# Kernel tuning notes

Hardware: AMD Instinct MI355X
Metric: run time of the kernel (lower is better)

## Reference

```python
import jax, jax.numpy as jnp
import numpy as np

# ---- hyperparameters (from args defaults) ----
TEMPERATURE = 0.07
ALPHA = 0.5
OT_EPSILON = 0.1
OT_ITERS = 20
HOLO_WEIGHT = 1.0
RKD_DISTANCE_WEIGHT = 1.0
RKD_ANGLE_WEIGHT = 2.0
GLOBAL_RKD_WEIGHT = 10.0
MATRYOSHKA_DIMS = [128, 768]
MATRYOSHKA_WEIGHTS = [1.0, 2.0]

B, N, H_S, H_T, D_REP = 64, 256, 768, 1024, 768


def l2norm(x, axis=-1):
    # F.normalize(p=2): x / max(||x||, eps)
    n = jnp.sqrt(jnp.sum(x * x, axis=axis, keepdims=True))
    return x / jnp.maximum(n, 1e-12)


def pairwise_distance(x):
    # [n, d] -> [n, n] squared-euclidean-style distances
    sq = jnp.sum(x * x, axis=1, keepdims=True)
    return sq + sq.T - 2.0 * (x @ x.T)


def huber(diff):
    a = jnp.abs(diff)
    return jnp.where(a < 1.0, 0.5 * a * a, a - 0.5)


def rkd_distance_loss(s, t):
    n = s.shape[0]
    mask = jnp.triu(jnp.ones((n, n), dtype=bool), k=1)
    cnt = jnp.sum(mask.astype(s.dtype))
    ds, dt = pairwise_distance(s), pairwise_distance(t)
    mean_s = jax.lax.stop_gradient(jnp.sum(jnp.where(mask, ds, 0.0)) / cnt) + 1e-8
    mean_t = jax.lax.stop_gradient(jnp.sum(jnp.where(mask, dt, 0.0)) / cnt) + 1e-8
    loss = huber(ds / mean_s - dt / mean_t)
    return jnp.sum(jnp.where(mask, loss, 0.0)) / cnt


def angle_potentials(x):
    # diffs[i, j] = x[j] - x[i]
    diffs = x[None, :, :] - x[:, None, :]
    e = diffs / (jnp.linalg.norm(diffs, axis=-1, keepdims=True) + 1e-8)
    return jnp.einsum('ijd,kjd->ijk', e, e)


def rkd_angle_loss(s, t):
    psi_s, psi_t = angle_potentials(s), angle_potentials(t)
    n = psi_s.shape[0]
    idx = jnp.arange(n)
    i, j, k = idx[:, None, None], idx[None, :, None], idx[None, None, :]
    mask = (i != j) & (i != k) & (j != k)  # exclude degenerate triplets
    cnt = jnp.sum(mask.astype(s.dtype))
    loss = huber(psi_s - psi_t)
    return jnp.sum(jnp.where(mask, loss, 0.0)) / cnt


def saliency_measure(h, temp=1.0):
    # softmax over token axis of hidden-state norms -> [B, N, 1]
    norms = jnp.linalg.norm(h, axis=-1)
    return jax.nn.softmax(norms / temp, axis=-1)[..., None]


def structure_matrix(z):
    zn = l2norm(z, axis=-1)
    return 1.0 - jnp.einsum('bnd,bmd->bnm', zn, zn)


def sinkhorn_knopp_log_domain(C, mu, nu):
    # C: [B, Ns, Nt]; mu: [B, Ns, 1]; nu: [B, Nt, 1]
    log_K = -C / OT_EPSILON
    log_mu = jnp.log(mu + 1e-8)
    log_nu = jnp.log(nu + 1e-8)
    u = jnp.zeros_like(mu)
    v = jnp.zeros_like(nu)
    for _ in range(OT_ITERS):
        u = log_mu - jax.scipy.special.logsumexp(
            log_K + jnp.swapaxes(v, 1, 2), axis=2, keepdims=True)
        v = log_nu - jax.scipy.special.logsumexp(
            jnp.swapaxes(log_K, 1, 2) + jnp.swapaxes(u, 1, 2),
            axis=2, keepdims=True)
    return jnp.exp(u + log_K + jnp.swapaxes(v, 1, 2))


def fused_gromov_wasserstein(z_s, z_t, proj_w, proj_b):
    mu = saliency_measure(z_s)   # [B, N, 1]
    nu = saliency_measure(z_t)   # [B, N, 1]
    C_s = structure_matrix(z_s)  # [B, N, N]
    C_t = structure_matrix(z_t)
    z_s_norm = l2norm(z_s @ proj_w + proj_b, axis=-1)
    z_t_norm = l2norm(z_t, axis=-1)
    M = 1.0 - jnp.einsum('bnd,bmd->bnm', z_s_norm, z_t_norm)
    Gamma = sinkhorn_knopp_log_domain(M, mu, nu)
    feat_loss = jnp.mean(jnp.sum(M * Gamma, axis=(1, 2)))
    Gamma_norm = Gamma / (jnp.sum(Gamma, axis=2, keepdims=True) + 1e-8)
    C_t_mapped = jnp.einsum('bnm,bmk,blk->bnl', Gamma_norm, C_t, Gamma_norm)
    w = jnp.einsum('bni,bmi->bnm', mu, mu)  # mu @ mu^T
    struct_loss = jnp.mean(jnp.sum((C_s - C_t_mapped) ** 2 * w, axis=(1, 2)))
    return (1.0 - ALPHA) * feat_loss + ALPHA * struct_loss


def cross_entropy_inbatch(scores):
    # labels = arange(B)
    logZ = jax.scipy.special.logsumexp(scores, axis=1)
    return jnp.mean(logZ - jnp.diagonal(scores))


def setup_inputs() -> dict:
    key = jax.random.key(0)
    ks = jax.random.split(key, 10)
    return {
        's_q_reps': jax.random.normal(ks[0], (B, D_REP), jnp.float32),
        's_p_reps': jax.random.normal(ks[1], (B, D_REP), jnp.float32),
        't_q_reps': jax.random.normal(ks[2], (B, D_REP), jnp.float32),
        't_p_reps': jax.random.normal(ks[3], (B, D_REP), jnp.float32),
        's_q_states': jax.random.normal(ks[4], (B, N, H_S), jnp.float32),
        's_p_states': jax.random.normal(ks[5], (B, N, H_S), jnp.float32),
        't_q_states': jax.random.normal(ks[6], (B, N, H_T), jnp.float32),
        't_p_states': jax.random.normal(ks[7], (B, N, H_T), jnp.float32),
        'proj_w': jax.random.normal(ks[8], (H_S, H_T), jnp.float32) * (H_S ** -0.5),
        'proj_b': jnp.zeros((H_T,), jnp.float32),
    }


def reference(s_q_reps, s_p_reps, t_q_reps, t_p_reps,
              s_q_states, s_p_states, t_q_states, t_p_states,
              proj_w, proj_b):
    # teacher outputs are computed under torch.no_grad()
    t_q_reps = jax.lax.stop_gradient(t_q_reps)
    t_p_reps = jax.lax.stop_gradient(t_p_reps)
    t_q_states = jax.lax.stop_gradient(t_q_states)
    t_p_states = jax.lax.stop_gradient(t_p_states)

    contrastive_acc = 0.0
    holo_acc = 0.0
    rkd_acc = 0.0
    for dim, dim_weight in zip(MATRYOSHKA_DIMS, MATRYOSHKA_WEIGHTS):
        s_q_slice = l2norm(s_q_reps[:, :dim])
        s_p_slice = l2norm(s_p_reps[:, :dim])
        scores = (s_q_slice @ s_p_slice.T) / TEMPERATURE
        contrastive_acc += dim_weight * cross_entropy_inbatch(scores)
        if dim <= 128:
            s_batch = jnp.concatenate([s_q_slice, s_p_slice], axis=0)
            t_batch = jnp.concatenate(
                [l2norm(t_q_reps[:, :dim]), l2norm(t_p_reps[:, :dim])], axis=0)
            loss_dist = rkd_distance_loss(s_batch, t_batch)
            loss_angle = rkd_angle_loss(s_batch, t_batch)
            rkd_val = (RKD_DISTANCE_WEIGHT * loss_dist
                       + RKD_ANGLE_WEIGHT * loss_angle)
            rkd_acc += GLOBAL_RKD_WEIGHT * rkd_val * 2.0
        else:
            loss_q = fused_gromov_wasserstein(s_q_states, t_q_states, proj_w, proj_b)
            loss_p = fused_gromov_wasserstein(s_p_states, t_p_states, proj_w, proj_b)
            holo_acc += HOLO_WEIGHT * 0.5 * (loss_q + loss_p)
    return contrastive_acc + holo_acc + rkd_acc
```

## Files before the change

kernel.cpp:

```cpp
#include <hip/hip_runtime.h>
#include <math.h>

#define NB   64
#define NN   256
#define HSS  768
#define HTT  1024
#define ROWS (NB*NN)
#define C2LOG 14.426950408889634f

typedef unsigned short u16;
typedef __attribute__((ext_vector_type(8))) short bf16x8;
typedef __attribute__((ext_vector_type(4))) float f32x4;

#define LIDX(r,c) (((r)<<8) + (((((c)>>3) + (r)) & 31)<<3) + ((c)&7))
#define EIDX(r,c) (((r)<<7) + (((((c)>>3) + (r)) & 15)<<3) + ((c)&7))

__device__ __forceinline__ void gl16(const u16* g, u16* l){
  __builtin_amdgcn_global_load_lds(
      (const __attribute__((address_space(1))) unsigned int*)g,
      (__attribute__((address_space(3))) unsigned int*)l,
      16, 0, 0);
}

static const size_t OFF_ACC   = 0;
static const size_t OFF_SQ128 = 16;
static const size_t OFF_SP128 = OFF_SQ128 + 64*128;
static const size_t OFF_TQ128 = OFF_SP128 + 64*128;
static const size_t OFF_TP128 = OFF_TQ128 + 64*128;
static const size_t OFF_SQ768 = OFF_TP128 + 64*128;
static const size_t OFF_SP768 = OFF_SQ768 + 64*768;
static const size_t OFF_DS    = OFF_SP768 + 64*768;
static const size_t OFF_DT    = OFF_DS + 128*128;
static const size_t OFF_CS    = OFF_DT + 128*128;
static const size_t OFF_MBF   = OFF_CS  + (size_t)2*NB*NN*NN;
static const size_t OFF_ZS_BF = OFF_MBF + (size_t)NB*NN*NN;
static const size_t OFF_ZT_BF = OFF_ZS_BF + (size_t)ROWS*HSS/2;
static const size_t OFF_WT_BF = OFF_ZT_BF + (size_t)ROWS*HTT/2;
static const size_t OFF_ZSP_BF= OFF_WT_BF + (size_t)HTT*HSS/2;
static const size_t OFF_GN_BF = OFF_ZSP_BF+ (size_t)ROWS*HTT/2;
static const size_t OFF_CT_BF = OFF_GN_BF + (size_t)NB*NN*NN;
static const size_t OFF_T_BF  = OFF_ZS_BF;
static const size_t OFF_NS    = OFF_CT_BF + (size_t)NB*NN*NN;
static const size_t OFF_NT    = OFF_NS + ROWS;
static const size_t OFF_NSP   = OFF_NT + ROWS;
static const size_t OFF_MU    = OFF_NSP + ROWS;
static const size_t OFF_NU    = OFF_MU + 2*ROWS;


__device__ __forceinline__ float wred_sum(float v){
  #pragma unroll
  for(int o=32;o>0;o>>=1) v += __shfl_xor(v,o,64);
  return v;
}
__device__ __forceinline__ float wred_max(float v){
  #pragma unroll
  for(int o=32;o>0;o>>=1) v = fmaxf(v, __shfl_xor(v,o,64));
  return v;
}
__device__ __forceinline__ u16 f2bf(float f){
  unsigned u = __float_as_uint(f);
  unsigned r = (u + 0x7fffu + ((u>>16)&1u)) >> 16;
  return (u16)r;
}
__device__ __forceinline__ float bf2f(u16 h){
  return __uint_as_float(((unsigned)h)<<16);
}

__global__ __launch_bounds__(256) void k_l2norm_all(
    const float* __restrict__ sq, const float* __restrict__ sp,
    const float* __restrict__ tq, const float* __restrict__ tp,
    float* __restrict__ ws){
  int bid = blockIdx.x;
  int r = bid & 63;
  const float* in; float* out; int kuse;
  if(bid < 64)       { in = sq; out = ws + OFF_SQ128; kuse = 128; }
  else if(bid < 128) { in = sp; out = ws + OFF_SP128; kuse = 128; }
  else if(bid < 192) { in = tq; out = ws + OFF_TQ128; kuse = 128; }
  else if(bid < 256) { in = tp; out = ws + OFF_TP128; kuse = 128; }
  else if(bid < 320) { in = sq; out = ws + OFF_SQ768; kuse = 768; }
  else               { in = sp; out = ws + OFF_SP768; kuse = 768; }
  const float* row = in + (size_t)r*768;
  float ss = 0.f;
  for(int d=threadIdx.x; d<kuse; d+=256){ float x=row[d]; ss += x*x; }
  ss = wred_sum(ss);
  __shared__ float sm[4];
  if((threadIdx.x&63)==0) sm[threadIdx.x>>6]=ss;
  __syncthreads();
  float tot = sm[0]+sm[1]+sm[2]+sm[3];
  float inv = 1.f / fmaxf(sqrtf(tot), 1e-12f);
  for(int d=threadIdx.x; d<kuse; d+=256) out[(size_t)r*kuse + d] = row[d]*inv;
}

__global__ __launch_bounds__(512) void k_contrastive2(const float* __restrict__ ws,
    float* __restrict__ acc){
  int bid = blockIdx.x;
  int i = bid & 63;
  int big = bid >> 6;
  const float* q = ws + (big ? OFF_SQ768 : OFF_SQ128);
  const float* p = ws + (big ? OFF_SP768 : OFF_SP128);
  int dim = big ? 768 : 128;
  float weight = big ? 2.f : 1.f;
  int j = threadIdx.x & 63;
  int part = threadIdx.x >> 6;
  const float* qi = q + (size_t)i*dim;
  const float* pj = p + (size_t)j*dim;
  int seg = dim >> 3;
  int d0 = part*seg;
  float dot = 0.f;
  for(int d=d0; d<d0+seg; d+=4){
    float4 a = *(const float4*)(qi+d);
    float4 b = *(const float4*)(pj+d);
    dot = fmaf(a.x,b.x,dot);
    dot = fmaf(a.y,b.y,dot);
    dot = fmaf(a.z,b.z,dot);
    dot = fmaf(a.w,b.w,dot);
  }
  __shared__ float sm[8][64];
  sm[part][j] = dot;
  __syncthreads();
  if(part==0){
    float s = 0.f;
    #pragma unroll
    for(int k=0;k<8;k++) s += sm[k][j];
    s = s / 0.07f;
    float mx = wred_max(s);
    float e = expf(s - mx);
    float Z = wred_sum(e);
    float logZ = mx + logf(Z);
    float diag = __shfl(s, i, 64);
    if(j==0) atomicAdd(acc+0, weight*(logZ - diag)*(1.f/64.f));
  }
}

__global__ __launch_bounds__(256) void k_pack_cvt(
    const float* __restrict__ zs, const float* __restrict__ zt,
    u16* __restrict__ zsb, u16* __restrict__ ztb,
    float* __restrict__ ns, float* __restrict__ nt,
    const float* __restrict__ sb128, const float* __restrict__ tb128,
    float* __restrict__ ds, float* __restrict__ dt, float* __restrict__ acc)
{
  __shared__ float sm[2][2];
  int bid = blockIdx.x;
  if(bid < 8192){
    const float* in; u16* out; float* nrm; int K; int cb;
    if(bid < 4096){ in=zs; out=zsb; nrm=ns; K=HSS; cb=bid; }
    else          { in=zt; out=ztb; nrm=nt; K=HTT; cb=bid-4096; }
    int w = threadIdx.x >> 6, l = threadIdx.x & 63;
    int r = cb*4 + w;
    const float* row = in + (size_t)r*K;
    u16* orow = out + (size_t)r*K;
    float ss = 0.f;
    int nv = K >> 8;
    for(int i=0;i<nv;i++){
      int d = l*4 + i*256;
      float4 x = *(const float4*)(row + d);
      ushort4 o; o.x=f2bf(x.x); o.y=f2bf(x.y); o.z=f2bf(x.z); o.w=f2bf(x.w);
      *(ushort4*)(orow + d) = o;
      ss += x.x*x.x + x.y*x.y + x.z*x.z + x.w*x.w;
    }
    ss = wred_sum(ss);
    if(l==0) nrm[r] = sqrtf(ss);
    return;
  }
  {
    int r = bid - 8192;
    int c = threadIdx.x;
    float ms = 0.f, mt = 0.f;
    if(c < 128){
      const float* sr = sb128 + r*128; const float* sc = sb128 + c*128;
      const float* tr = tb128 + r*128; const float* tc = tb128 + c*128;
      float dot_s=0,ssr=0,ssc=0,dot_t=0,tsr=0,tsc=0;
      for(int d=0; d<128; d++){
        float a=sr[d], bb=sc[d]; dot_s += a*bb; ssr += a*a; ssc += bb*bb;
        float at=tr[d], bt=tc[d]; dot_t += at*bt; tsr += at*at; tsc += bt*bt;
      }
      float dv = ssr + ssc - 2.f*dot_s;
      float tv = tsr + tsc - 2.f*dot_t;
      ds[r*128+c] = dv; dt[r*128+c] = tv;
      ms = (c>r)? dv : 0.f;
      mt = (c>r)? tv : 0.f;
      ms = wred_sum(ms); mt = wred_sum(mt);
      if((c&63)==0){ sm[0][c>>6]=ms; sm[1][c>>6]=mt; }
    }
    __syncthreads();
    if(threadIdx.x==0){
      atomicAdd(acc+1, sm[0][0]+sm[0][1]);
      atomicAdd(acc+2, sm[1][0]+sm[1][1]);
    }
  }
}

__global__ __launch_bounds__(256) void k_small0(
    const float* __restrict__ ds, const float* __restrict__ dt,
    const float* __restrict__ ns, const float* __restrict__ nt,
    float* __restrict__ omu, float* __restrict__ onu, float* __restrict__ acc)
{
  __shared__ float sm[4], sm2[4];
  int bid = blockIdx.x;
  if(bid < 128){
    int r = bid, c = threadIdx.x;
    float mean_s = acc[1]*(1.f/8128.f) + 1e-8f;
    float mean_t = acc[2]*(1.f/8128.f) + 1e-8f;
    float h = 0.f;
    if(c < 128){
      if(c > r){
        float diff = ds[r*128+c]/mean_s - dt[r*128+c]/mean_t;
        float a = fabsf(diff);
        h = (a<1.f)? 0.5f*a*a : a-0.5f;
      }
      h = wred_sum(h);
      if((c&63)==0) sm[c>>6]=h;
    }
    __syncthreads();
    if(threadIdx.x==0) atomicAdd(acc+3, sm[0]+sm[1]);
    return;
  }
  {
    int b0 = bid - 128, n = threadIdx.x;
    const float* nrm = (b0 < NB) ? ns : nt;
    float* out = (b0 < NB) ? omu : onu;
    int b = b0 & 63;
    float x = nrm[b*NN+n];
    float mx = wred_max(x);
    if((n&63)==0) sm[n>>6]=mx;
    __syncthreads();
    mx = fmaxf(fmaxf(sm[0],sm[1]),fmaxf(sm[2],sm[3]));
    float e = expf(x-mx);
    float s = wred_sum(e);
    if((n&63)==0) sm2[n>>6]=s;
    __syncthreads();
    s = sm2[0]+sm2[1]+sm2[2]+sm2[3];
    out[b*NN+n] = e/s;
  }
}

#define RKD_LDS 65536
__global__ __launch_bounds__(256, 1) void k_rkd_angle_mfma(
    const float* __restrict__ sb, const float* __restrict__ tb,
    float* __restrict__ accp)
{
  extern __shared__ u16 eSh[];
  u16* Es = eSh;
  u16* Et = eSh + 128*128;
  const int j    = blockIdx.x >> 1;
  const int half = blockIdx.x & 1;
  const int tid = threadIdx.x;
  {
    const int i = tid >> 1, h = tid & 1;
    #pragma unroll
    for(int which=0; which<2; which++){
      const float* xb = which ? tb : sb;
      u16* E = which ? Et : Es;
      const float* xj = xb + j*128 + h*64;
      const float* xi = xb + i*128 + h*64;
      float ss = 0.f;
      #pragma unroll
      for(int d4=0; d4<16; d4++){
        float4 a = *(const float4*)(xj + d4*4);
        float4 b = *(const float4*)(xi + d4*4);
        float d0=a.x-b.x, d1=a.y-b.y, d2=a.z-b.z, d3=a.w-b.w;
        ss += d0*d0+d1*d1+d2*d2+d3*d3;
      }
      ss += __shfl_xor(ss, 1, 64);
      float inv = (i==j) ? 0.f : 1.f/(sqrtf(ss)+1e-8f);
      #pragma unroll
      for(int d4=0; d4<16; d4++){
        float4 a = *(const float4*)(xj + d4*4);
        float4 b = *(const float4*)(xi + d4*4);
        int c = h*64 + d4*4;
        E[EIDX(i,c+0)] = f2bf((a.x-b.x)*inv);
        E[EIDX(i,c+1)] = f2bf((a.y-b.y)*inv);
        E[EIDX(i,c+2)] = f2bf((a.z-b.z)*inv);
        E[EIDX(i,c+3)] = f2bf((a.w-b.w)*inv);
      }
    }
  }
  __syncthreads();
  const int w = tid >> 6, lane = tid & 63;
  const int q = lane >> 4, loc = lane & 15;
  float hsum = 0.f;
  #pragma unroll
  for(int ni=0; ni<4; ni++){
    const int cb = half*64 + ni*16;
    #pragma unroll
    for(int mi=0; mi<2; mi++){
      const int rb = w*32 + mi*16;
      f32x4 as_ = {0.f,0.f,0.f,0.f}, at_ = {0.f,0.f,0.f,0.f};
      #pragma unroll
      for(int k0=0; k0<128; k0+=32){
        int ra = rb + loc, rbn = cb + loc;
        int ca = k0 + q*8;
        bf16x8 aS = *(const bf16x8*)(Es + EIDX(ra, ca));
        bf16x8 bS = *(const bf16x8*)(Es + EIDX(rbn, ca));
        bf16x8 aT = *(const bf16x8*)(Et + EIDX(ra, ca));
        bf16x8 bT = *(const bf16x8*)(Et + EIDX(rbn, ca));
        as_ = __builtin_amdgcn_mfma_f32_16x16x32_bf16(aS, bS, as_, 0,0,0);
        at_ = __builtin_amdgcn_mfma_f32_16x16x32_bf16(aT, bT, at_, 0,0,0);
      }
      #pragma unroll
      for(int jj=0; jj<4; jj++){
        int row = rb + q*4 + jj, col = cb + loc;
        if(row != col){
          float d = as_[jj] - at_[jj];
          float a = fabsf(d);
          hsum += (a < 1.f) ? 0.5f*a*a : a - 0.5f;
        }
      }
    }
  }
  hsum = wred_sum(hsum);
  __syncthreads();
  float* red = (float*)eSh;
  if(lane==0) red[w] = hsum;
  __syncthreads();
  if(tid==0) atomicAdd(accp+4, red[0]+red[1]+red[2]+red[3]);
}

__global__ __launch_bounds__(256) void k_row_norm_bf16(const u16* __restrict__ z,
    float* __restrict__ nrm, int K){
  int w = threadIdx.x >> 6, l = threadIdx.x & 63;
  int r = blockIdx.x*4 + w;
  const u16* row = z + (size_t)r*K;
  float ss = 0.f;
  int nv = K >> 9;
  for(int i=0;i<nv;i++){
    int d = l*8 + i*512;
    uint4 v = *(const uint4*)(row + d);
    float a0=__uint_as_float(v.x<<16), a1=__uint_as_float(v.x&0xffff0000u);
    float a2=__uint_as_float(v.y<<16), a3=__uint_as_float(v.y&0xffff0000u);
    float a4=__uint_as_float(v.z<<16), a5=__uint_as_float(v.z&0xffff0000u);
    float a6=__uint_as_float(v.w<<16), a7=__uint_as_float(v.w&0xffff0000u);
    ss += a0*a0+a1*a1+a2*a2+a3*a3+a4*a4+a5*a5+a6*a6+a7*a7;
  }
  ss = wred_sum(ss);
  if(l==0) nrm[r] = sqrtf(ss);
}

__global__ void k_wt(const float* __restrict__ W, u16* __restrict__ Wt){
  __shared__ float t[32][33];
  int k0 = blockIdx.y*32, n0 = blockIdx.x*32;
  int tx = threadIdx.x, ty = threadIdx.y;
  for(int r=0;r<32;r+=8) t[ty+r][tx] = W[(size_t)(k0+ty+r)*HTT + n0+tx];
  __syncthreads();
  for(int r=0;r<32;r+=8) Wt[(size_t)(n0+ty+r)*HSS + k0+tx] = f2bf(t[tx][ty+r]);
}

__global__ __launch_bounds__(256) void k_saliency2(const float* __restrict__ ns,
    const float* __restrict__ nt, float* __restrict__ omu, float* __restrict__ onu){
  int b0 = blockIdx.x, n = threadIdx.x;
  const float* nrm = (b0 < NB) ? ns : nt;
  float* out = (b0 < NB) ? omu : onu;
  int b = b0 & 63;
  float x = nrm[b*NN+n];
  float mx = wred_max(x);
  __shared__ float sm[4], sm2[4];
  if((n&63)==0) sm[n>>6]=mx;
  __syncthreads();
  mx = fmaxf(fmaxf(sm[0],sm[1]),fmaxf(sm[2],sm[3]));
  float e = expf(x-mx);
  float s = wred_sum(e);
  if((n&63)==0) sm2[n>>6]=s;
  __syncthreads();
  s = sm2[0]+sm2[1]+sm2[2]+sm2[3];
  out[b*NN+n] = e/s;
}

enum { MODE_PROJ=0, MODE_COST=1, MODE_PLAIN=2, MODE_STRUCT=3 };

template<int MODE>
__global__ __launch_bounds__(256) void k_mfma(
    const u16* __restrict__ A, int lda, long bA,
    const u16* __restrict__ B, int ldb, long bB,
    int K,
    float* __restrict__ outF, u16* __restrict__ outB, int ldo, long bO,
    const float* __restrict__ nx, const float* __restrict__ ny,
    const float* __restrict__ bias,
    const float* __restrict__ Cs, const float* __restrict__ mu,
    float* __restrict__ accp)
{
  __shared__ u16 As[128*32];
  __shared__ u16 Bs[128*32];
  __shared__ float red[4];

  int gx = gridDim.x, gy = gridDim.y;
  int flat = blockIdx.x + gx*(blockIdx.y + gy*blockIdx.z);
  int nwg  = gx*gy*gridDim.z;
  int cpx  = nwg >> 3;
  int lg   = (flat & 7)*cpx + (flat >> 3);
  int bx   = lg % gx;
  int rest = lg / gx;
  int by   = rest % gy;
  int b    = rest / gy;

  const u16* Ab = A + (size_t)b*bA;
  const u16* Bb = B + (size_t)b*bB;
  int tid = threadIdx.x;
  int lane = tid & 63, w = tid >> 6;
  int m0 = by*128, n0 = bx*128;
  int row_off = (w>>1)*64, col_off = (w&1)*64;
  int q = lane>>4, loc = lane&15;
  f32x4 acc[4][4] = {};

  const int srow = (lane >> 2);
  const int sslot = lane & 3;

  for(int k0=0;k0<K;k0+=32){
    #pragma unroll
    for(int h=0;h<2;h++){
      int row = h*64 + w*16 + srow;
      int ca  = (sslot ^ ((row>>1)&3))*8;
      u16* ldst = As + h*2048 + w*512 + lane*8;
      u16* ldstB= Bs + h*2048 + w*512 + lane*8;
      gl16(Ab + (size_t)(m0+row)*lda + k0 + ca, ldst);
      gl16(Bb + (size_t)(n0+row)*ldb + k0 + ca, ldstB);
    }
    __syncthreads();
    bf16x8 af[4], bfr[4];
    #pragma unroll
    for(int mi=0;mi<4;mi++){
      int r = row_off + mi*16 + loc;
      int slot = q ^ ((r>>1)&3);
      af[mi] = *(const bf16x8*)(As + r*32 + slot*8);
    }
    #pragma unroll
    for(int ni=0;ni<4;ni++){
      int r = col_off + ni*16 + loc;
      int slot = q ^ ((r>>1)&3);
      bfr[ni] = *(const bf16x8*)(Bs + r*32 + slot*8);
    }
    #pragma unroll
    for(int mi=0;mi<4;mi++)
      #pragma unroll
      for(int ni=0;ni<4;ni++)
        acc[mi][ni] = __builtin_amdgcn_mfma_f32_16x16x32_bf16(af[mi], bfr[ni], acc[mi][ni], 0,0,0);
    __syncthreads();
  }

  float* outFb = outF ? outF + (size_t)b*bO : nullptr;
  u16*   outBb = outB ? outB + (size_t)b*bO : nullptr;
  const float* nxb = nx ? nx + (size_t)b*NN : nullptr;
  const float* nyb = ny ? ny + (size_t)b*NN : nullptr;
  const float* Cb  = (MODE==MODE_STRUCT) ? Cs + (size_t)b*bO : nullptr;
  const float* mb  = (MODE==MODE_STRUCT) ? mu + (size_t)b*NN : nullptr;
  float lsum = 0.f;
  #pragma unroll
  for(int mi=0;mi<4;mi++){
    #pragma unroll
    for(int j=0;j<4;j++){
      int row = m0 + row_off + mi*16 + q*4 + j;
      float ir = 0.f, mr = 0.f;
      if(MODE==MODE_COST)   ir = 1.f/fmaxf(nxb[row],1e-12f);
      if(MODE==MODE_STRUCT) mr = mb[row];
      #pragma unroll
      for(int ni=0;ni<4;ni++){
        int col = n0 + col_off + ni*16 + loc;
        float v = acc[mi][ni][j];
        if(MODE==MODE_PROJ){
          v += bias[col];
          outBb[(size_t)row*ldo + col] = f2bf(v);
        } else if(MODE==MODE_COST){
          float ic = 1.f/fmaxf(nyb[col],1e-12f);
          v = 1.f - v*ir*ic;
          if(outFb) outFb[(size_t)row*ldo + col] = v;
          if(outBb) outBb[(size_t)row*ldo + col] = f2bf(v);
        } else if(MODE==MODE_PLAIN){
          outBb[(size_t)row*ldo + col] = f2bf(v);
        } else {
          float d = Cb[(size_t)row*ldo + col] - v;
          lsum += d*d*mr*mb[col];
        }
      }
    }
  }
  if(MODE==MODE_STRUCT){
    lsum = wred_sum(lsum);
    if(lane==0) red[w] = lsum;
    __syncthreads();
    if(tid==0) atomicAdd(accp+6, red[0]+red[1]+red[2]+red[3]);
  }
}

template<int MODE>
__global__ __launch_bounds__(256) void k_mfma64(
    const u16* __restrict__ A, int lda, long bA,
    const u16* __restrict__ B, int ldb, long bB,
    int K,
    float* __restrict__ outF, u16* __restrict__ outB, int ldo, long bO,
    const float* __restrict__ nx, const float* __restrict__ ny,
    const float* __restrict__ bias,
    const float* __restrict__ Cs, const float* __restrict__ mu,
    float* __restrict__ accp)
{
  __shared__ u16 As[64*32];
  __shared__ u16 Bs[64*32];
  __shared__ float red[4];

  int gx = gridDim.x, gy = gridDim.y;
  int flat = blockIdx.x + gx*(blockIdx.y + gy*blockIdx.z);
  int nwg  = gx*gy*gridDim.z;
  int cpx  = nwg >> 3;
  int lg   = (flat & 7)*cpx + (flat >> 3);
  int bx   = lg % gx;
  int rest = lg / gx;
  int by   = rest % gy;
  int b    = rest / gy;

  const u16* Ab = A + (size_t)b*bA;
  const u16* Bb = B + (size_t)b*bB;
  int tid = threadIdx.x;
  int lane = tid & 63, w = tid >> 6;
  int m0 = by*64, n0 = bx*64;
  int row_off = (w>>1)*32, col_off = (w&1)*32;
  int q = lane>>4, loc = lane&15;
  f32x4 acc[2][2] = {};

  const int srow = tid >> 2;
  const int sslot = tid & 3;

  for(int k0=0;k0<K;k0+=32){
    {
      int row = srow;
      int ca  = (sslot ^ ((row>>1)&3))*8;
      u16* la = As + w*512 + lane*8;
      u16* lb = Bs + w*512 + lane*8;
      gl16(Ab + (size_t)(m0+row)*lda + k0 + ca, la);
      gl16(Bb + (size_t)(n0+row)*ldb + k0 + ca, lb);
    }
    __syncthreads();
    bf16x8 af[2], bfr[2];
    #pragma unroll
    for(int mi=0;mi<2;mi++){
      int r = row_off + mi*16 + loc;
      int slot = q ^ ((r>>1)&3);
      af[mi] = *(const bf16x8*)(As + r*32 + slot*8);
    }
    #pragma unroll
    for(int ni=0;ni<2;ni++){
      int r = col_off + ni*16 + loc;
      int slot = q ^ ((r>>1)&3);
      bfr[ni] = *(const bf16x8*)(Bs + r*32 + slot*8);
    }
    #pragma unroll
    for(int mi=0;mi<2;mi++)
      #pragma unroll
      for(int ni=0;ni<2;ni++)
        acc[mi][ni] = __builtin_amdgcn_mfma_f32_16x16x32_bf16(af[mi], bfr[ni], acc[mi][ni], 0,0,0);
    __syncthreads();
  }

  float* outFb = outF ? outF + (size_t)b*bO : nullptr;
  u16*   outBb = outB ? outB + (size_t)b*bO : nullptr;
  const float* nxb = nx ? nx + (size_t)b*NN : nullptr;
  const float* nyb = ny ? ny + (size_t)b*NN : nullptr;
  const float* Cb  = (MODE==MODE_STRUCT) ? Cs + (size_t)b*bO : nullptr;
  const float* mb  = (MODE==MODE_STRUCT) ? mu + (size_t)b*NN : nullptr;
  float lsum = 0.f;
  #pragma unroll
  for(int mi=0;mi<2;mi++){
    #pragma unroll
    for(int j=0;j<4;j++){
      int row = m0 + row_off + mi*16 + q*4 + j;
      float ir = 0.f, mr = 0.f;
      if(MODE==MODE_COST)   ir = 1.f/fmaxf(nxb[row],1e-12f);
      if(MODE==MODE_STRUCT) mr = mb[row];
      #pragma unroll
      for(int ni=0;ni<2;ni++){
        int col = n0 + col_off + ni*16 + loc;
        float v = acc[mi][ni][j];
        if(MODE==MODE_PROJ){
          v += bias[col];
          outBb[(size_t)row*ldo + col] = f2bf(v);
        } else if(MODE==MODE_COST){
          float ic = 1.f/fmaxf(nyb[col],1e-12f);
          v = 1.f - v*ir*ic;
          if(outFb) outFb[(size_t)row*ldo + col] = v;
          if(outBb) outBb[(size_t)row*ldo + col] = f2bf(v);
        } else if(MODE==MODE_PLAIN){
          outBb[(size_t)row*ldo + col] = f2bf(v);
        } else {
          float d = Cb[(size_t)row*ldo + col] - v;
          lsum += d*d*mr*mb[col];
        }
      }
    }
  }
  if(MODE==MODE_STRUCT){
    lsum = wred_sum(lsum);
    if(lane==0) red[w] = lsum;
    __syncthreads();
    if(tid==0) atomicAdd(accp+6, red[0]+red[1]+red[2]+red[3]);
  }
}

__global__ __launch_bounds__(256) void k_mfma64_dual(
    const u16* __restrict__ A1, const u16* __restrict__ A2,
    const u16* __restrict__ B, int ld, long bStr,
    int K,
    u16* __restrict__ out1, u16* __restrict__ out2, long bO,
    const float* __restrict__ n1, const float* __restrict__ n2,
    const float* __restrict__ ny)
{
  __shared__ u16 A1s[64*32];
  __shared__ u16 A2s[64*32];
  __shared__ u16 Bs[64*32];

  int gx = gridDim.x, gy = gridDim.y;
  int flat = blockIdx.x + gx*(blockIdx.y + gy*blockIdx.z);
  int nwg  = gx*gy*gridDim.z;
  int cpx  = nwg >> 3;
  int lg   = (flat & 7)*cpx + (flat >> 3);
  int bx   = lg % gx;
  int rest = lg / gx;
  int by   = rest % gy;
  int b    = rest / gy;

  const u16* A1b = A1 + (size_t)b*bStr;
  const u16* A2b = A2 + (size_t)b*bStr;
  const u16* Bb  = B  + (size_t)b*bStr;
  int tid = threadIdx.x;
  int lane = tid & 63, w = tid >> 6;
  int m0 = by*64, n0 = bx*64;
  int row_off = (w>>1)*32, col_off = (w&1)*32;
  int q = lane>>4, loc = lane&15;
  f32x4 acc1[2][2] = {};
  f32x4 acc2[2][2] = {};

  const int srow = tid >> 2;
  const int sslot = tid & 3;

  for(int k0=0;k0<K;k0+=32){
    {
      int row = srow;
      int ca  = (sslot ^ ((row>>1)&3))*8;
      u16* l1 = A1s + w*512 + lane*8;
      u16* l2 = A2s + w*512 + lane*8;
      u16* lb = Bs  + w*512 + lane*8;
      gl16(A1b + (size_t)(m0+row)*ld + k0 + ca, l1);
      gl16(A2b + (size_t)(m0+row)*ld + k0 + ca, l2);
      gl16(Bb  + (size_t)(n0+row)*ld + k0 + ca, lb);
    }
    __syncthreads();
    bf16x8 a1f[2], a2f[2], bfr[2];
    #pragma unroll
    for(int mi=0;mi<2;mi++){
      int r = row_off + mi*16 + loc;
      int slot = q ^ ((r>>1)&3);
      a1f[mi] = *(const bf16x8*)(A1s + r*32 + slot*8);
      a2f[mi] = *(const bf16x8*)(A2s + r*32 + slot*8);
    }
    #pragma unroll
    for(int ni=0;ni<2;ni++){
      int r = col_off + ni*16 + loc;
      int slot = q ^ ((r>>1)&3);
      bfr[ni] = *(const bf16x8*)(Bs + r*32 + slot*8);
    }
    #pragma unroll
    for(int mi=0;mi<2;mi++)
      #pragma unroll
      for(int ni=0;ni<2;ni++){
        acc1[mi][ni] = __builtin_amdgcn_mfma_f32_16x16x32_bf16(a1f[mi], bfr[ni], acc1[mi][ni], 0,0,0);
        acc2[mi][ni] = __builtin_amdgcn_mfma_f32_16x16x32_bf16(a2f[mi], bfr[ni], acc2[mi][ni], 0,0,0);
      }
    __syncthreads();
  }

  u16* o1 = out1 + (size_t)b*bO;
  u16* o2 = out2 + (size_t)b*bO;
  const float* n1b = n1 + (size_t)b*NN;
  const float* n2b = n2 + (size_t)b*NN;
  const float* nyb = ny + (size_t)b*NN;
  #pragma unroll
  for(int mi=0;mi<2;mi++){
    #pragma unroll
    for(int j=0;j<4;j++){
      int row = m0 + row_off + mi*16 + q*4 + j;
      float ir1 = 1.f/fmaxf(n1b[row],1e-12f);
      float ir2 = 1.f/fmaxf(n2b[row],1e-12f);
      #pragma unroll
      for(int ni=0;ni<2;ni++){
        int col = n0 + col_off + ni*16 + loc;
        float ic = 1.f/fmaxf(nyb[col],1e-12f);
        float v1 = 1.f - acc1[mi][ni][j]*ir1*ic;
        float v2 = 1.f - acc2[mi][ni][j]*ir2*ic;
        o1[(size_t)row*NN + col] = f2bf(v1);
        o2[(size_t)row*NN + col] = f2bf(v2);
      }
    }
  }
}

#define SINK_DYN_LDS 131072
__global__ __launch_bounds__(1024, 1) void k_sinkhorn_fused(
    const u16* __restrict__ Mbf, const float* __restrict__ muL,
    const float* __restrict__ nuL, u16* __restrict__ Gn, float* __restrict__ accp)
{
  extern __shared__ u16 Ks[];
  __shared__ __align__(16) float part[4096];
  __shared__ __align__(16) float su[NN], sv[NN], smu[NN], snu[NN];
  __shared__ float red[16];

  const int b = blockIdx.x;
  const int t = threadIdx.x;
  const u16* Mb = Mbf + (size_t)b*NN*NN;

  #pragma unroll
  for(int i=0;i<16;i++){
    int e = (i*1024 + t)*4;
    int r = e>>8, c = e&255;
    ushort4 mv = *(const ushort4*)(Mb + e);
    ushort4 o;
    o.x = f2bf(exp2f(-C2LOG*bf2f(mv.x)));
    o.y = f2bf(exp2f(-C2LOG*bf2f(mv.y)));
    o.z = f2bf(exp2f(-C2LOG*bf2f(mv.z)));
    o.w = f2bf(exp2f(-C2LOG*bf2f(mv.w)));
    *(ushort4*)(Ks + LIDX(r,c)) = o;
  }
  if(t < NN){
    smu[t] = muL[(size_t)b*NN+t] + 1e-8f;
    snu[t] = nuL[(size_t)b*NN+t] + 1e-8f;
    sv[t] = 1.f;
  }
  __syncthreads();

  const int r_ = t & 255, p_ = t >> 8;
  const int w = t>>6, l = t&63;

  for(int it=0; it<20; it++){
    {
      float s0=0.f, s1=0.f, s2=0.f, s3=0.f;
      #pragma unroll
      for(int jj=0;jj<8;jj++){
        int c0 = p_*64 + jj*8;
        uint4 kv = *(const uint4*)(Ks + LIDX(r_, c0));
        float4 va = *(const float4*)(sv + c0);
        float4 vb = *(const float4*)(sv + c0 + 4);
        s0 = fmaf(__uint_as_float(kv.x<<16),           va.x, s0);
        s1 = fmaf(__uint_as_float(kv.x & 0xffff0000u), va.y, s1);
        s2 = fmaf(__uint_as_float(kv.y<<16),           va.z, s2);
        s3 = fmaf(__uint_as_float(kv.y & 0xffff0000u), va.w, s3);
        s0 = fmaf(__uint_as_float(kv.z<<16),           vb.x, s0);
        s1 = fmaf(__uint_as_float(kv.z & 0xffff0000u), vb.y, s1);
        s2 = fmaf(__uint_as_float(kv.w<<16),           vb.z, s2);
        s3 = fmaf(__uint_as_float(kv.w & 0xffff0000u), vb.w, s3);
      }
      part[t] = (s0+s1)+(s2+s3);
    }
    __syncthreads();
    if(t < NN){
      float S = part[t] + part[256+t] + part[512+t] + part[768+t];
      su[t] = smu[t] / S;
    }
    __syncthreads();
    {
      float cs0=0.f,cs1=0.f,cs2=0.f,cs3=0.f;
      #pragma unroll
      for(int rr=0;rr<16;rr++){
        int r = w*16 + rr;
        ushort4 kv = *(const ushort4*)(Ks + LIDX(r, l*4));
        float ur = su[r];
        cs0 = fmaf(bf2f(kv.x), ur, cs0);
        cs1 = fmaf(bf2f(kv.y), ur, cs1);
        cs2 = fmaf(bf2f(kv.z), ur, cs2);
        cs3 = fmaf(bf2f(kv.w), ur, cs3);
      }
      float4 o; o.x=cs0; o.y=cs1; o.z=cs2; o.w=cs3;
      *(float4*)(part + w*256 + l*4) = o;
    }
    __syncthreads();
    if(t < NN){
      float S = 0.f;
      #pragma unroll
      for(int ww=0;ww<16;ww++) S += part[ww*256 + t];
      sv[t] = snu[t] / S;
    }
    __syncthreads();
  }

  {
    float s0=0.f, s1=0.f, s2=0.f, s3=0.f;
    #pragma unroll
    for(int jj=0;jj<8;jj++){
      int c0 = p_*64 + jj*8;
      uint4 kv = *(const uint4*)(Ks + LIDX(r_, c0));
      float4 va = *(const float4*)(sv + c0);
      float4 vb = *(const float4*)(sv + c0 + 4);
      s0 = fmaf(__uint_as_float(kv.x<<16),           va.x, s0);
      s1 = fmaf(__uint_as_float(kv.x & 0xffff0000u), va.y, s1);
      s2 = fmaf(__uint_as_float(kv.y<<16),           va.z, s2);
      s3 = fmaf(__uint_as_float(kv.y & 0xffff0000u), va.w, s3);
      s0 = fmaf(__uint_as_float(kv.z<<16),           vb.x, s0);
      s1 = fmaf(__uint_as_float(kv.z & 0xffff0000u), vb.y, s1);
      s2 = fmaf(__uint_as_float(kv.w<<16),           vb.z, s2);
      s3 = fmaf(__uint_as_float(kv.w & 0xffff0000u), vb.w, s3);
    }
    part[t] = (s0+s1)+(s2+s3);
  }
  __syncthreads();
  if(t < NN){
    float S = part[t] + part[256+t] + part[512+t] + part[768+t];
    smu[t] = 1.f / (su[t]*S + 1e-8f);
  }
  __syncthreads();

  u16* Gb = Gn + (size_t)b*NN*NN;
  const float IC = -1.f/C2LOG;
  float v0 = sv[l*4+0], v1 = sv[l*4+1], v2 = sv[l*4+2], v3 = sv[l*4+3];
  float fl = 0.f;
  for(int rr=0;rr<16;rr++){
    int r = w*16 + rr;
    ushort4 kv = *(const ushort4*)(Ks + LIDX(r, l*4));
    float k0=bf2f(kv.x), k1=bf2f(kv.y), k2=bf2f(kv.z), k3=bf2f(kv.w);
    float ur = su[r], inv = smu[r];
    float g0=ur*k0*v0, g1=ur*k1*v1, g2=ur*k2*v2, g3=ur*k3*v3;
    fl += g0*(__log2f(k0)*IC) + g1*(__log2f(k1)*IC)
        + g2*(__log2f(k2)*IC) + g3*(__log2f(k3)*IC);
    ushort4 o;
    o.x=f2bf(g0*inv); o.y=f2bf(g1*inv); o.z=f2bf(g2*inv); o.w=f2bf(g3*inv);
    *(ushort4*)(Gb + (size_t)r*NN + l*4) = o;
  }
  fl = wred_sum(fl);
  if(l==0) red[w] = fl;
  __syncthreads();
  if(t==0){
    float s=0.f;
    #pragma unroll
    for(int i=0;i<16;i++) s+=red[i];
    atomicAdd(accp+5, s);
  }
}

__global__ void k_final(const float* __restrict__ acc, float* __restrict__ out){
  out[0] = acc[0]
         + 20.f*acc[3]*(1.f/8128.f)
         + 40.f*acc[4]*(1.f/2048256.f)
         + 0.25f*(acc[5]+acc[6])*(1.f/64.f);
}

extern "C" void kernel_launch(void* const* d_in, const int* in_sizes, int n_in,
                              void* d_out, int out_size, void* d_ws, size_t ws_size,
                              hipStream_t stream) {
  const float* s_q_reps   = (const float*)d_in[0];
  const float* s_p_reps   = (const float*)d_in[1];
  const float* t_q_reps   = (const float*)d_in[2];
  const float* t_p_reps   = (const float*)d_in[3];
  const float* s_q_states = (const float*)d_in[4];
  const float* s_p_states = (const float*)d_in[5];
  const float* t_q_states = (const float*)d_in[6];
  const float* t_p_states = (const float*)d_in[7];
  const float* proj_w     = (const float*)d_in[8];
  const float* proj_b     = (const float*)d_in[9];
  float* ws = (float*)d_ws;
  float* acc = ws + OFF_ACC;
  u16* M_BF   = (u16*)(ws + OFF_MBF);
  u16* ZS_BF  = (u16*)(ws + OFF_ZS_BF);
  u16* ZT_BF  = (u16*)(ws + OFF_ZT_BF);
  u16* WT_BF  = (u16*)(ws + OFF_WT_BF);
  u16* ZSP_BF = (u16*)(ws + OFF_ZSP_BF);
  u16* GN_BF  = (u16*)(ws + OFF_GN_BF);
  u16* CT_BF  = (u16*)(ws + OFF_CT_BF);
  u16* T_BF   = (u16*)(ws + OFF_T_BF);

  hipFuncSetAttribute(reinterpret_cast<const void*>(k_sinkhorn_fused),
                      hipFuncAttributeMaxDynamicSharedMemorySize, SINK_DYN_LDS);
  hipFuncSetAttribute(reinterpret_cast<const void*>(k_rkd_angle_mfma),
                      hipFuncAttributeMaxDynamicSharedMemorySize, RKD_LDS);

  hipMemsetAsync(acc, 0, 16*sizeof(float), stream);

  k_l2norm_all<<<384,256,0,stream>>>(s_q_reps, s_p_reps, t_q_reps, t_p_reps, ws);
  k_contrastive2<<<128,512,0,stream>>>(ws, acc);

  k_pack_cvt<<<8320,256,0,stream>>>(s_q_states, t_q_states, ZS_BF, ZT_BF,
      ws+OFF_NS, ws+OFF_NT, ws+OFF_SQ128, ws+OFF_TQ128, ws+OFF_DS, ws+OFF_DT, acc);
  k_small0<<<256,256,0,stream>>>(ws+OFF_DS, ws+OFF_DT, ws+OFF_NS, ws+OFF_NT,
      ws+OFF_MU, ws+OFF_NU, acc);
  k_rkd_angle_mfma<<<256,256,RKD_LDS,stream>>>(ws+OFF_SQ128, ws+OFF_TQ128, acc);
  k_wt<<<dim3(HTT/32, HSS/32),dim3(32,8),0,stream>>>(proj_w, WT_BF);

  for(int pass=0; pass<2; pass++){
    size_t po  = (size_t)pass*NB*NN*NN;
    size_t pr  = (size_t)pass*ROWS;
    if(pass==1){
      k_pack_cvt<<<8192,256,0,stream>>>(s_p_states, t_p_states, ZS_BF, ZT_BF,
          ws+OFF_NS, ws+OFF_NT, ws+OFF_SQ128, ws+OFF_TQ128, ws+OFF_DS, ws+OFF_DT, acc);
      k_saliency2<<<128,256,0,stream>>>(ws+OFF_NS, ws+OFF_NT, ws+OFF_MU+pr, ws+OFF_NU+pr);
    }
    k_mfma<MODE_PROJ><<<dim3(HTT/128, ROWS/128, 1),256,0,stream>>>(
        ZS_BF, HSS, 0, WT_BF, HSS, 0, HSS,
        nullptr, ZSP_BF, HTT, 0,
        nullptr, nullptr, proj_b, nullptr, nullptr, nullptr);
    k_row_norm_bf16<<<ROWS/4,256,0,stream>>>(ZSP_BF, ws+OFF_NSP, HTT);
    k_mfma64<MODE_COST><<<dim3(4,4,NB),256,0,stream>>>(
        ZS_BF, HSS, (long)NN*HSS, ZS_BF, HSS, (long)NN*HSS, HSS,
        ws+OFF_CS+po, nullptr, NN, (long)NN*NN,
        ws+OFF_NS, ws+OFF_NS, nullptr, nullptr, nullptr, nullptr);
    k_mfma64_dual<<<dim3(4,4,NB),256,0,stream>>>(
        ZT_BF, ZSP_BF, ZT_BF, HTT, (long)NN*HTT, HTT,
        CT_BF+po, M_BF+po, (long)NN*NN,
        ws+OFF_NT, ws+OFF_NSP, ws+OFF_NT);
  }

  k_sinkhorn_fused<<<2*NB,1024,SINK_DYN_LDS,stream>>>(
      M_BF, ws+OFF_MU, ws+OFF_NU, GN_BF, acc);

  k_mfma64<MODE_PLAIN><<<dim3(4,4,2*NB),256,0,stream>>>(
      GN_BF, NN, (long)NN*NN, CT_BF, NN, (long)NN*NN, NN,
      nullptr, T_BF, NN, (long)NN*NN,
      nullptr, nullptr, nullptr, nullptr, nullptr, nullptr);
  k_mfma64<MODE_STRUCT><<<dim3(4,4,2*NB),256,0,stream>>>(
      T_BF, NN, (long)NN*NN, GN_BF, NN, (long)NN*NN, NN,
      nullptr, nullptr, NN, (long)NN*NN,
      nullptr, nullptr, nullptr, ws+OFF_CS, ws+OFF_MU, acc);

  k_final<<<1,1,0,stream>>>(acc, (float*)d_out);
}
```

Measured before the change: 603.1 us.

## Fuse projection row norms into projection GEMM and overlap pass-1 cost GEMM with Sinkhorn

The projection GEMM now writes per-slice partial sums of squares of its bf16 outputs, which replaces the separate row-norm kernel. The dual GEMM sums the 16 partials to get each row norm. The pass-1 student cost-matrix GEMM moves into extra blocks of the Sinkhorn launch (384 blocks instead of 128), so it runs alongside the 128 Sinkhorn blocks rather than as its own launch. The intent is to drop a kernel launch and a re-read of the projected matrix, and to fill idle CUs during Sinkhorn. The cost is that 1024-thread blocks with large LDS doing small GEMMs may use those CUs inefficiently.

```diff
diff --git a/kernel.cpp b/kernel.cpp
--- a/kernel.cpp
+++ b/kernel.cpp
@@ -42,9 +42,9 @@
 static const size_t OFF_T_BF  = OFF_ZS_BF;
 static const size_t OFF_NS    = OFF_CT_BF + (size_t)NB*NN*NN;
 static const size_t OFF_NT    = OFF_NS + ROWS;
-static const size_t OFF_NSP   = OFF_NT + ROWS;
-static const size_t OFF_MU    = OFF_NSP + ROWS;
+static const size_t OFF_MU    = OFF_NT + ROWS;
 static const size_t OFF_NU    = OFF_MU + 2*ROWS;
+static const size_t OFF_NSPP  = OFF_NU + 2*ROWS;
 
 
 __device__ __forceinline__ float wred_sum(float v){
@@ -316,26 +316,6 @@
   if(tid==0) atomicAdd(accp+4, red[0]+red[1]+red[2]+red[3]);
 }
 
-__global__ __launch_bounds__(256) void k_row_norm_bf16(const u16* __restrict__ z,
-    float* __restrict__ nrm, int K){
-  int w = threadIdx.x >> 6, l = threadIdx.x & 63;
-  int r = blockIdx.x*4 + w;
-  const u16* row = z + (size_t)r*K;
-  float ss = 0.f;
-  int nv = K >> 9;
-  for(int i=0;i<nv;i++){
-    int d = l*8 + i*512;
-    uint4 v = *(const uint4*)(row + d);
-    float a0=__uint_as_float(v.x<<16), a1=__uint_as_float(v.x&0xffff0000u);
-    float a2=__uint_as_float(v.y<<16), a3=__uint_as_float(v.y&0xffff0000u);
-    float a4=__uint_as_float(v.z<<16), a5=__uint_as_float(v.z&0xffff0000u);
-    float a6=__uint_as_float(v.w<<16), a7=__uint_as_float(v.w&0xffff0000u);
-    ss += a0*a0+a1*a1+a2*a2+a3*a3+a4*a4+a5*a5+a6*a6+a7*a7;
-  }
-  ss = wred_sum(ss);
-  if(l==0) nrm[r] = sqrtf(ss);
-}
-
 __global__ void k_wt(const float* __restrict__ W, u16* __restrict__ Wt){
   __shared__ float t[32][33];
   int k0 = blockIdx.y*32, n0 = blockIdx.x*32;
@@ -365,35 +345,22 @@
   out[b*NN+n] = e/s;
 }
 
-enum { MODE_PROJ=0, MODE_COST=1, MODE_PLAIN=2, MODE_STRUCT=3 };
-
-template<int MODE>
-__global__ __launch_bounds__(256) void k_mfma(
-    const u16* __restrict__ A, int lda, long bA,
-    const u16* __restrict__ B, int ldb, long bB,
-    int K,
-    float* __restrict__ outF, u16* __restrict__ outB, int ldo, long bO,
-    const float* __restrict__ nx, const float* __restrict__ ny,
-    const float* __restrict__ bias,
-    const float* __restrict__ Cs, const float* __restrict__ mu,
-    float* __restrict__ accp)
+__global__ __launch_bounds__(256) void k_proj(
+    const u16* __restrict__ A, const u16* __restrict__ B,
+    u16* __restrict__ outB, const float* __restrict__ bias,
+    float* __restrict__ nspp)
 {
   __shared__ u16 As[128*32];
   __shared__ u16 Bs[128*32];
-  __shared__ float red[4];
 
   int gx = gridDim.x, gy = gridDim.y;
-  int flat = blockIdx.x + gx*(blockIdx.y + gy*blockIdx.z);
-  int nwg  = gx*gy*gridDim.z;
+  int flat = blockIdx.x + gx*blockIdx.y;
+  int nwg  = gx*gy;
   int cpx  = nwg >> 3;
   int lg   = (flat & 7)*cpx + (flat >> 3);
   int bx   = lg % gx;
-  int rest = lg / gx;
-  int by   = rest % gy;
-  int b    = rest / gy;
-
-  const u16* Ab = A + (size_t)b*bA;
-  const u16* Bb = B + (size_t)b*bB;
+  int by   = lg / gx;
+
   int tid = threadIdx.x;
   int lane = tid & 63, w = tid >> 6;
   int m0 = by*128, n0 = bx*128;
@@ -404,15 +371,15 @@
   const int srow = (lane >> 2);
   const int sslot = lane & 3;
 
-  for(int k0=0;k0<K;k0+=32){
+  for(int k0=0;k0<HSS;k0+=32){
     #pragma unroll
     for(int h=0;h<2;h++){
       int row = h*64 + w*16 + srow;
       int ca  = (sslot ^ ((row>>1)&3))*8;
       u16* ldst = As + h*2048 + w*512 + lane*8;
       u16* ldstB= Bs + h*2048 + w*512 + lane*8;
-      gl16(Ab + (size_t)(m0+row)*lda + k0 + ca, ldst);
-      gl16(Bb + (size_t)(n0+row)*ldb + k0 + ca, ldstB);
+      gl16(A + (size_t)(m0+row)*HSS + k0 + ca, ldst);
+      gl16(B + (size_t)(n0+row)*HSS + k0 + ca, ldstB);
     }
     __syncthreads();
     bf16x8 af[4], bfr[4];
@@ -436,49 +403,32 @@
     __syncthreads();
   }
 
-  float* outFb = outF ? outF + (size_t)b*bO : nullptr;
-  u16*   outBb = outB ? outB + (size_t)b*bO : nullptr;
-  const float* nxb = nx ? nx + (size_t)b*NN : nullptr;
-  const float* nyb = ny ? ny + (size_t)b*NN : nullptr;
-  const float* Cb  = (MODE==MODE_STRUCT) ? Cs + (size_t)b*bO : nullptr;
-  const float* mb  = (MODE==MODE_STRUCT) ? mu + (size_t)b*NN : nullptr;
-  float lsum = 0.f;
+  int slice = bx*2 + (w&1);
   #pragma unroll
   for(int mi=0;mi<4;mi++){
     #pragma unroll
     for(int j=0;j<4;j++){
       int row = m0 + row_off + mi*16 + q*4 + j;
-      float ir = 0.f, mr = 0.f;
-      if(MODE==MODE_COST)   ir = 1.f/fmaxf(nxb[row],1e-12f);
-      if(MODE==MODE_STRUCT) mr = mb[row];
+      float sq = 0.f;
       #pragma unroll
       for(int ni=0;ni<4;ni++){
         int col = n0 + col_off + ni*16 + loc;
-        float v = acc[mi][ni][j];
-        if(MODE==MODE_PROJ){
-          v += bias[col];
-          outBb[(size_t)row*ldo + col] = f2bf(v);
-        } else if(MODE==MODE_COST){
-          float ic = 1.f/fmaxf(nyb[col],1e-12f);
-          v = 1.f - v*ir*ic;
-          if(outFb) outFb[(size_t)row*ldo + col] = v;
-          if(outBb) outBb[(size_t)row*ldo + col] = f2bf(v);
-        } else if(MODE==MODE_PLAIN){
-          outBb[(size_t)row*ldo + col] = f2bf(v);
-        } else {
-          float d = Cb[(size_t)row*ldo + col] - v;
-          lsum += d*d*mr*mb[col];
-        }
-      }
-    }
-  }
-  if(MODE==MODE_STRUCT){
-    lsum = wred_sum(lsum);
-    if(lane==0) red[w] = lsum;
-    __syncthreads();
-    if(tid==0) atomicAdd(accp+6, red[0]+red[1]+red[2]+red[3]);
-  }
-}
+        float v = acc[mi][ni][j] + bias[col];
+        u16 h = f2bf(v);
+        outB[(size_t)row*HTT + col] = h;
+        float vq = bf2f(h);
+        sq = fmaf(vq, vq, sq);
+      }
+      sq += __shfl_xor(sq, 1, 64);
+      sq += __shfl_xor(sq, 2, 64);
+      sq += __shfl_xor(sq, 4, 64);
+      sq += __shfl_xor(sq, 8, 64);
+      if(loc==0) nspp[(size_t)slice*ROWS + row] = sq;
+    }
+  }
+}
+
+enum { MODE_PROJ=0, MODE_COST=1, MODE_PLAIN=2, MODE_STRUCT=3 };
 
 template<int MODE>
 __global__ __launch_bounds__(256) void k_mfma64(
@@ -567,17 +517,14 @@
       for(int ni=0;ni<2;ni++){
         int col = n0 + col_off + ni*16 + loc;
         float v = acc[mi][ni][j];
-        if(MODE==MODE_PROJ){
-          v += bias[col];
-          outBb[(size_t)row*ldo + col] = f2bf(v);
-        } else if(MODE==MODE_COST){
+        if(MODE==MODE_COST){
           float ic = 1.f/fmaxf(nyb[col],1e-12f);
           v = 1.f - v*ir*ic;
           if(outFb) outFb[(size_t)row*ldo + col] = v;
           if(outBb) outBb[(size_t)row*ldo + col] = f2bf(v);
         } else if(MODE==MODE_PLAIN){
           outBb[(size_t)row*ldo + col] = f2bf(v);
-        } else {
+        } else if(MODE==MODE_STRUCT){
           float d = Cb[(size_t)row*ldo + col] - v;
           lsum += d*d*mr*mb[col];
         }
@@ -597,7 +544,7 @@
     const u16* __restrict__ B, int ld, long bStr,
     int K,
     u16* __restrict__ out1, u16* __restrict__ out2, long bO,
-    const float* __restrict__ n1, const float* __restrict__ n2,
+    const float* __restrict__ n1, const float* __restrict__ nspp,
     const float* __restrict__ ny)
 {
   __shared__ u16 A1s[64*32];
@@ -667,7 +614,6 @@
   u16* o1 = out1 + (size_t)b*bO;
   u16* o2 = out2 + (size_t)b*bO;
   const float* n1b = n1 + (size_t)b*NN;
-  const float* n2b = n2 + (size_t)b*NN;
   const float* nyb = ny + (size_t)b*NN;
   #pragma unroll
   for(int mi=0;mi<2;mi++){
@@ -675,7 +621,11 @@
     for(int j=0;j<4;j++){
       int row = m0 + row_off + mi*16 + q*4 + j;
       float ir1 = 1.f/fmaxf(n1b[row],1e-12f);
-      float ir2 = 1.f/fmaxf(n2b[row],1e-12f);
+      size_t gr = (size_t)b*NN + row;
+      float ssq = 0.f;
+      #pragma unroll
+      for(int s=0;s<16;s++) ssq += nspp[(size_t)s*ROWS + gr];
+      float ir2 = 1.f/fmaxf(sqrtf(ssq),1e-12f);
       #pragma unroll
       for(int ni=0;ni<2;ni++){
         int col = n0 + col_off + ni*16 + loc;
@@ -690,17 +640,87 @@
 }
 
 #define SINK_DYN_LDS 131072
-__global__ __launch_bounds__(1024, 1) void k_sinkhorn_fused(
+__global__ __launch_bounds__(1024, 1) void k_sink_cs(
     const u16* __restrict__ Mbf, const float* __restrict__ muL,
-    const float* __restrict__ nuL, u16* __restrict__ Gn, float* __restrict__ accp)
+    const float* __restrict__ nuL, u16* __restrict__ Gn, float* __restrict__ accp,
+    const u16* __restrict__ ZS, const float* __restrict__ ns,
+    float* __restrict__ CsOut)
 {
-  extern __shared__ u16 Ks[];
+  extern __shared__ u16 dynLds[];
   __shared__ __align__(16) float part[4096];
   __shared__ __align__(16) float su[NN], sv[NN], smu[NN], snu[NN];
   __shared__ float red[16];
 
-  const int b = blockIdx.x;
+  const int bid = blockIdx.x;
   const int t = threadIdx.x;
+
+  if(bid >= 128){
+    const int sub = t >> 8;
+    const int st  = t & 255;
+    int job = (bid - 128)*4 + sub;
+    int bx = job & 3, by = (job >> 2) & 3, b = job >> 4;
+    const u16* Ab = ZS + (size_t)b*NN*HSS;
+    u16* As = dynLds + (size_t)sub*4096;
+    u16* Bs = As + 2048;
+    int lane = st & 63, w = st >> 6;
+    int m0 = by*64, n0 = bx*64;
+    int row_off = (w>>1)*32, col_off = (w&1)*32;
+    int q = lane>>4, loc = lane&15;
+    f32x4 acc[2][2] = {};
+    const int srow = st >> 2;
+    const int sslot = st & 3;
+
+    for(int k0=0;k0<HSS;k0+=32){
+      {
+        int row = srow;
+        int ca  = (sslot ^ ((row>>1)&3))*8;
+        gl16(Ab + (size_t)(m0+row)*HSS + k0 + ca, As + w*512 + lane*8);
+        gl16(Ab + (size_t)(n0+row)*HSS + k0 + ca, Bs + w*512 + lane*8);
+      }
+      __syncthreads();
+      bf16x8 af[2], bfr[2];
+      #pragma unroll
+      for(int mi=0;mi<2;mi++){
+        int r = row_off + mi*16 + loc;
+        int slot = q ^ ((r>>1)&3);
+        af[mi] = *(const bf16x8*)(As + r*32 + slot*8);
+      }
+      #pragma unroll
+      for(int ni=0;ni<2;ni++){
+        int r = col_off + ni*16 + loc;
+        int slot = q ^ ((r>>1)&3);
+        bfr[ni] = *(const bf16x8*)(Bs + r*32 + slot*8);
+      }
+      #pragma unroll
+      for(int mi=0;mi<2;mi++)
+        #pragma unroll
+        for(int ni=0;ni<2;ni++)
+          acc[mi][ni] = __builtin_amdgcn_mfma_f32_16x16x32_bf16(af[mi], bfr[ni], acc[mi][ni], 0,0,0);
+      __syncthreads();
+    }
+
+    float* outFb = CsOut + (size_t)b*NN*NN;
+    const float* nb = ns + (size_t)b*NN;
+    #pragma unroll
+    for(int mi=0;mi<2;mi++){
+      #pragma unroll
+      for(int j=0;j<4;j++){
+        int row = m0 + row_off + mi*16 + q*4 + j;
+        float ir = 1.f/fmaxf(nb[row],1e-12f);
+        #pragma unroll
+        for(int ni=0;ni<2;ni++){
+          int col = n0 + col_off + ni*16 + loc;
+          float ic = 1.f/fmaxf(nb[col],1e-12f);
+          float v = 1.f - acc[mi][ni][j]*ir*ic;
+          outFb[(size_t)row*NN + col] = v;
+        }
+      }
+    }
+    return;
+  }
+
+  u16* Ks = dynLds;
+  const int b = bid;
   const u16* Mb = Mbf + (size_t)b*NN*NN;
 
   #pragma unroll
@@ -860,7 +880,7 @@
   u16* CT_BF  = (u16*)(ws + OFF_CT_BF);
   u16* T_BF   = (u16*)(ws + OFF_T_BF);
 
-  hipFuncSetAttribute(reinterpret_cast<const void*>(k_sinkhorn_fused),
+  hipFuncSetAttribute(reinterpret_cast<const void*>(k_sink_cs),
                       hipFuncAttributeMaxDynamicSharedMemorySize, SINK_DYN_LDS);
   hipFuncSetAttribute(reinterpret_cast<const void*>(k_rkd_angle_mfma),
                       hipFuncAttributeMaxDynamicSharedMemorySize, RKD_LDS);
@@ -885,23 +905,23 @@
           ws+OFF_NS, ws+OFF_NT, ws+OFF_SQ128, ws+OFF_TQ128, ws+OFF_DS, ws+OFF_DT, acc);
       k_saliency2<<<128,256,0,stream>>>(ws+OFF_NS, ws+OFF_NT, ws+OFF_MU+pr, ws+OFF_NU+pr);
     }
-    k_mfma<MODE_PROJ><<<dim3(HTT/128, ROWS/128, 1),256,0,stream>>>(
-        ZS_BF, HSS, 0, WT_BF, HSS, 0, HSS,
-        nullptr, ZSP_BF, HTT, 0,
-        nullptr, nullptr, proj_b, nullptr, nullptr, nullptr);
-    k_row_norm_bf16<<<ROWS/4,256,0,stream>>>(ZSP_BF, ws+OFF_NSP, HTT);
-    k_mfma64<MODE_COST><<<dim3(4,4,NB),256,0,stream>>>(
-        ZS_BF, HSS, (long)NN*HSS, ZS_BF, HSS, (long)NN*HSS, HSS,
-        ws+OFF_CS+po, nullptr, NN, (long)NN*NN,
-        ws+OFF_NS, ws+OFF_NS, nullptr, nullptr, nullptr, nullptr);
+    k_proj<<<dim3(HTT/128, ROWS/128),256,0,stream>>>(
+        ZS_BF, WT_BF, ZSP_BF, proj_b, ws+OFF_NSPP);
+    if(pass==0){
+      k_mfma64<MODE_COST><<<dim3(4,4,NB),256,0,stream>>>(
+          ZS_BF, HSS, (long)NN*HSS, ZS_BF, HSS, (long)NN*HSS, HSS,
+          ws+OFF_CS+po, nullptr, NN, (long)NN*NN,
+          ws+OFF_NS, ws+OFF_NS, nullptr, nullptr, nullptr, nullptr);
+    }
     k_mfma64_dual<<<dim3(4,4,NB),256,0,stream>>>(
         ZT_BF, ZSP_BF, ZT_BF, HTT, (long)NN*HTT, HTT,
         CT_BF+po, M_BF+po, (long)NN*NN,
-        ws+OFF_NT, ws+OFF_NSP, ws+OFF_NT);
-  }
-
-  k_sinkhorn_fused<<<2*NB,1024,SINK_DYN_LDS,stream>>>(
-      M_BF, ws+OFF_MU, ws+OFF_NU, GN_BF, acc);
+        ws+OFF_NT, ws+OFF_NSPP, ws+OFF_NT);
+  }
+
+  k_sink_cs<<<384,1024,SINK_DYN_LDS,stream>>>(
+      M_BF, ws+OFF_MU, ws+OFF_NU, GN_BF, acc,
+      ZS_BF, ws+OFF_NS, ws+OFF_CS + (size_t)NB*NN*NN);
 
   k_mfma64<MODE_PLAIN><<<dim3(4,4,2*NB),256,0,stream>>>(
       GN_BF, NN, (long)NN*NN, CT_BF, NN, (long)NN*NN, NN,
```

After: 590.3 us. 2.1% less time.
